# Kernel tuning notes

Measured on AMD Instinct MI355X. Metric: run time of the kernel, lower is better.

Reference implementation:

```python
import jax, jax.numpy as jnp
import numpy as np

B, N, D = 4, 2048, 1024


def setup_inputs() -> dict:
    key = jax.random.key(0)
    ks = jax.random.split(key, 9)
    x = jax.random.normal(ks[0], (B, N, D), dtype=jnp.float32)
    # causal mask: True = masked (set to -inf), per dot_product_attention semantics
    mask = jnp.triu(jnp.ones((N, N), dtype=bool), k=1)
    mask = jnp.broadcast_to(mask, (B, N, N))
    scale = 1.0 / np.sqrt(D)
    Wq = jax.random.normal(ks[1], (D, D), dtype=jnp.float32) * scale
    Wk = jax.random.normal(ks[2], (D, D), dtype=jnp.float32) * scale
    Wv = jax.random.normal(ks[3], (D, D), dtype=jnp.float32) * scale
    Wo = jax.random.normal(ks[4], (D, D), dtype=jnp.float32) * scale
    bq = jnp.zeros((D,), dtype=jnp.float32)
    bk = jnp.zeros((D,), dtype=jnp.float32)
    bv = jnp.zeros((D,), dtype=jnp.float32)
    bo = jnp.zeros((D,), dtype=jnp.float32)
    return {"x": x, "mask": mask, "Wq": Wq, "bq": bq, "Wk": Wk, "bk": bk,
            "Wv": Wv, "bv": bv, "Wo": Wo, "bo": bo}


def reference(x, mask, Wq, bq, Wk, bk, Wv, bv, Wo, bo):
    # QKV projections (single-head despite docstring; module never splits heads)
    Q = x @ Wq + bq  # [b, n, d]
    K = x @ Wk + bk
    V = x @ Wv + bv
    d = K.shape[-1]
    scores = jnp.einsum('bqd,bkd->bqk', Q, K) / jnp.sqrt(jnp.asarray(d, Q.dtype))
    min_infty = jnp.finfo(scores.dtype).min
    scores = jnp.where(mask, min_infty, scores)
    weights = jax.nn.softmax(scores, axis=-1)
    attention = jnp.einsum('bqk,bkd->bqd', weights, V)
    out = attention @ Wo + bo
    return out
```

## Files before the change

### kernel.cpp

```cpp
#include <hip/hip_runtime.h>
#include <hip/hip_bf16.h>

typedef __attribute__((ext_vector_type(8))) short short8;
typedef __attribute__((ext_vector_type(4))) float f32x4;

__device__ inline float b2f(unsigned short u) {
    union { unsigned int i; float f; } c; c.i = ((unsigned int)u) << 16; return c.f;
}
__device__ inline unsigned short f2b(float f) {
    __hip_bfloat16 h = __float2bfloat16(f);
    return *reinterpret_cast<unsigned short*>(&h);
}

__device__ inline void gl_lds16(const unsigned short* g, unsigned short* ldsbase) {
    __builtin_amdgcn_global_load_lds(
        (const __attribute__((address_space(1))) unsigned int*)(g),
        (__attribute__((address_space(3))) unsigned int*)(ldsbase),
        16, 0, 0);
}

__global__ __launch_bounds__(256) void cvt_f32_bf16(
    const float* __restrict__ src, unsigned short* __restrict__ dst, int n4)
{
    int i = blockIdx.x * 256 + threadIdx.x;
    if (i >= n4) return;
    float4 v = ((const float4*)src)[i];
    union { unsigned short u[4]; unsigned long long ll; } p;
    p.u[0] = f2b(v.x); p.u[1] = f2b(v.y); p.u[2] = f2b(v.z); p.u[3] = f2b(v.w);
    ((unsigned long long*)dst)[i] = p.ll;
}

__global__ __launch_bounds__(256) void cvt_weights4(
    const float* __restrict__ s0, const float* __restrict__ s1, const float* __restrict__ s2,
    const float* __restrict__ s3,
    unsigned short* __restrict__ d0, unsigned short* __restrict__ d1,
    unsigned short* __restrict__ d2, unsigned short* __restrict__ d3)
{
    const int z = blockIdx.z;
    if (z == 3) {
        const int i = (blockIdx.y * 32 + blockIdx.x) * 256 + threadIdx.x;
        float4 v = ((const float4*)s3)[i];
        union { unsigned short u[4]; unsigned long long ll; } p;
        p.u[0] = f2b(v.x); p.u[1] = f2b(v.y); p.u[2] = f2b(v.z); p.u[3] = f2b(v.w);
        ((unsigned long long*)d3)[i] = p.ll;
        return;
    }
    const float* src = z == 0 ? s0 : z == 1 ? s1 : s2;
    unsigned short* dst = z == 0 ? d0 : z == 1 ? d1 : d2;
    __shared__ float tile[32][33];
    const int c0 = blockIdx.x * 32, r0 = blockIdx.y * 32;
    const int tx = threadIdx.x & 31, ty = threadIdx.x >> 5;
    #pragma unroll
    for (int i = ty; i < 32; i += 8)
        tile[i][tx] = src[(long)(r0 + i) * 1024 + c0 + tx];
    __syncthreads();
    #pragma unroll
    for (int i = ty; i < 32; i += 8)
        dst[(long)(c0 + i) * 1024 + r0 + tx] = f2b(tile[tx][i]);
}

__global__ __launch_bounds__(64) void make_bvo(
    const unsigned short* __restrict__ Wot, const float* __restrict__ bv,
    const float* __restrict__ bo, float* __restrict__ bvo)
{
    const int n = blockIdx.x;
    const int lane = threadIdx.x;
    const unsigned short* row = Wot + (long)n * 1024;
    float acc = 0.f;
    #pragma unroll
    for (int pass = 0; pass < 2; pass++) {
        const int k = pass * 512 + lane * 8;
        short8 wv = *(const short8*)(row + k);
        #pragma unroll
        for (int j = 0; j < 8; j++)
            acc += bv[k + j] * b2f((unsigned short)wv[j]);
    }
    #pragma unroll
    for (int off = 32; off > 0; off >>= 1) acc += __shfl_xor(acc, off, 64);
    if (lane == 0) bvo[n] = acc + bo[n];
}

#define TILE_DECLS \
    __shared__ __attribute__((aligned(16))) unsigned short As[2 * 128 * 32]; \
    __shared__ __attribute__((aligned(16))) unsigned short Bs[2 * 128 * 32]; \
    const int t = threadIdx.x, lane = t & 63, w = t >> 6; \
    const int wr = w >> 1, wc = w & 1; \
    const int lrow = lane & 15, quad = lane >> 4; \
    f32x4 acc[4][4]; \
    _Pragma("unroll") for (int i = 0; i < 4; i++) \
        _Pragma("unroll") for (int j = 0; j < 4; j++) \
            acc[i][j] = (f32x4){0.f, 0.f, 0.f, 0.f};

#define TILE_KLOOP(gA, lda, gB, ldb, Keff) \
    for (int k0 = 0; k0 < (Keff); k0 += 64) { \
        _Pragma("unroll") for (int p = 0; p < 2; p++) \
            _Pragma("unroll") for (int h = 0; h < 2; h++) { \
                gl_lds16((gA) + (long)h * 16 * (lda) + k0 + p * 32, \
                         &As[p * 4096 + (w * 32 + h * 16) * 32]); \
                gl_lds16((gB) + (long)h * 16 * (ldb) + k0 + p * 32, \
                         &Bs[p * 4096 + (w * 32 + h * 16) * 32]); \
            } \
        __syncthreads(); \
        _Pragma("unroll") for (int p = 0; p < 2; p++) { \
            short8 af[4], bfr[4]; \
            _Pragma("unroll") for (int mi = 0; mi < 4; mi++) \
                af[mi] = *(const short8*)&As[p * 4096 + (wr * 64 + mi * 16 + lrow) * 32 + quad * 8]; \
            _Pragma("unroll") for (int ni = 0; ni < 4; ni++) \
                bfr[ni] = *(const short8*)&Bs[p * 4096 + (wc * 64 + ni * 16 + lrow) * 32 + quad * 8]; \
            _Pragma("unroll") for (int mi = 0; mi < 4; mi++) \
                _Pragma("unroll") for (int ni = 0; ni < 4; ni++) \
                    acc[mi][ni] = __builtin_amdgcn_mfma_f32_16x16x32_bf16( \
                        af[mi], bfr[ni], acc[mi][ni], 0, 0, 0); \
        } \
        __syncthreads(); \
    }

__global__ __launch_bounds__(256) void qkv_proj(
    const unsigned short* __restrict__ A,
    const unsigned short* __restrict__ Wqt, const unsigned short* __restrict__ Wkt,
    const unsigned short* __restrict__ Wvot,
    const float* __restrict__ bq, const float* __restrict__ bk,
    unsigned short* __restrict__ Q, unsigned short* __restrict__ Km,
    unsigned short* __restrict__ Vot)
{
    const int bm = blockIdx.x, bn = blockIdx.y;
    const int r = bn >> 3, bnn = bn & 7;
    const unsigned short* Bt = (r == 0) ? Wqt : (r == 1) ? Wkt : Wvot;
    const float* bias = (r == 0) ? bq : (r == 1) ? bk : nullptr;
    const int m0 = bm * 128, n0 = bnn * 128;

    TILE_DECLS

    const unsigned short* gA = A  + (long)(m0 + w * 32 + (lane >> 2)) * 1024 + (lane & 3) * 8;
    const unsigned short* gB = Bt + (long)(n0 + w * 32 + (lane >> 2)) * 1024 + (lane & 3) * 8;
    TILE_KLOOP(gA, 1024, gB, 1024, 1024)

    #pragma unroll
    for (int mi = 0; mi < 4; mi++) {
        const int m = m0 + wr * 64 + mi * 16 + quad * 4;
        #pragma unroll
        for (int ni = 0; ni < 4; ni++) {
            const int n = n0 + wc * 64 + ni * 16 + lrow;
            const float bvl = bias ? bias[n] : 0.f;
            if (r < 2) {
                unsigned short* out = (r == 0) ? Q : Km;
                #pragma unroll
                for (int rg = 0; rg < 4; rg++)
                    out[(long)(m + rg) * 1024 + n] = f2b(acc[mi][ni][rg] + bvl);
            } else {
                #pragma unroll
                for (int rg = 0; rg < 4; rg++)
                    Vot[(long)n * 8192 + m + rg] = f2b(acc[mi][ni][rg]);
            }
        }
    }
}

template<bool TRI, bool KCAUSAL, int OMODE>
__global__ __launch_bounds__(256) void gemm128(
    const unsigned short* __restrict__ A, const unsigned short* __restrict__ Bt,
    const float* __restrict__ bias, void* __restrict__ Cv,
    int K, int lda, int ldb, int ldc, long sA, long sB, long sC, float scale)
{
    int bm, bn, bz;
    if (TRI) {
        const int q = blockIdx.x;
        bm = (int)((sqrtf(8.f * q + 1.f) - 1.f) * 0.5f);
        while ((bm + 1) * (bm + 2) / 2 <= q) bm++;
        while (bm * (bm + 1) / 2 > q) bm--;
        bn = q - bm * (bm + 1) / 2;
        bz = blockIdx.y;
    } else {
        bm = KCAUSAL ? (gridDim.x - 1 - blockIdx.x) : blockIdx.x;
        bn = blockIdx.y; bz = blockIdx.z;
    }
    A  += (long)bz * sA;
    Bt += (long)bz * sB;
    const int m0 = bm * 128, n0 = bn * 128;

    TILE_DECLS

    const int Keff = KCAUSAL ? ((bm + 1) * 128 < K ? (bm + 1) * 128 : K) : K;
    const unsigned short* gA = A  + (long)(m0 + w * 32 + (lane >> 2)) * lda + (lane & 3) * 8;
    const unsigned short* gB = Bt + (long)(n0 + w * 32 + (lane >> 2)) * ldb + (lane & 3) * 8;
    TILE_KLOOP(gA, lda, gB, ldb, Keff)

    #pragma unroll
    for (int mi = 0; mi < 4; mi++) {
        const int m = m0 + wr * 64 + mi * 16 + quad * 4;
        #pragma unroll
        for (int ni = 0; ni < 4; ni++) {
            const int n = n0 + wc * 64 + ni * 16 + lrow;
            const float bvl = bias ? bias[n] : 0.f;
            #pragma unroll
            for (int rg = 0; rg < 4; rg++) {
                const float val = acc[mi][ni][rg] * scale + bvl;
                if (OMODE == 1)
                    ((float*)Cv)[(long)bz * sC + (long)(m + rg) * ldc + n] = val;
                else
                    ((unsigned short*)Cv)[(long)bz * sC + (long)(m + rg) * ldc + n] = f2b(val);
            }
        }
    }
}

__global__ __launch_bounds__(256) void softmax_causal(unsigned short* __restrict__ S)
{
    const long row = blockIdx.x;
    const int i = (int)(row & 2047);
    unsigned short* base = S + row * 2048;
    const int t = threadIdx.x;
    const int padded = ((i >> 7) + 1) << 7;
    const int j0 = t * 8;
    const bool active = j0 < padded;

    __shared__ float red[4];

    float v[8];
    if (active) {
        short8 s8 = *(const short8*)(base + j0);
        #pragma unroll
        for (int jj = 0; jj < 8; jj++)
            v[jj] = (j0 + jj <= i) ? b2f((unsigned short)s8[jj]) : -3.0e38f;
    } else {
        #pragma unroll
        for (int jj = 0; jj < 8; jj++) v[jj] = -3.0e38f;
    }

    float lmax = v[0];
    #pragma unroll
    for (int jj = 1; jj < 8; jj++) lmax = fmaxf(lmax, v[jj]);
    #pragma unroll
    for (int off = 32; off > 0; off >>= 1) lmax = fmaxf(lmax, __shfl_xor(lmax, off, 64));
    if ((t & 63) == 0) red[t >> 6] = lmax;
    __syncthreads();
    const float gmax = fmaxf(fmaxf(red[0], red[1]), fmaxf(red[2], red[3]));
    __syncthreads();

    float lsum = 0.f;
    #pragma unroll
    for (int jj = 0; jj < 8; jj++) {
        v[jj] = (v[jj] > -1.0e37f) ? __expf(v[jj] - gmax) : 0.f;
        lsum += v[jj];
    }
    #pragma unroll
    for (int off = 32; off > 0; off >>= 1) lsum += __shfl_xor(lsum, off, 64);
    if ((t & 63) == 0) red[t >> 6] = lsum;
    __syncthreads();
    const float inv = 1.0f / (red[0] + red[1] + red[2] + red[3]);

    if (active) {
        short8 p8;
        #pragma unroll
        for (int jj = 0; jj < 8; jj++) p8[jj] = (short)f2b(v[jj] * inv);
        *(short8*)(base + j0) = p8;
    }
}

extern "C" void kernel_launch(void* const* d_in, const int* in_sizes, int n_in,
                              void* d_out, int out_size, void* d_ws, size_t ws_size,
                              hipStream_t stream)
{
    const float* x  = (const float*)d_in[0];
    const float* Wq = (const float*)d_in[2];
    const float* bq = (const float*)d_in[3];
    const float* Wk = (const float*)d_in[4];
    const float* bk = (const float*)d_in[5];
    const float* Wv = (const float*)d_in[6];
    const float* bv = (const float*)d_in[7];
    const float* Wo = (const float*)d_in[8];
    const float* bo = (const float*)d_in[9];

    unsigned short* ws = (unsigned short*)d_ws;
    const long XSZ = 8192L * 1024;
    const long WSZ = 1024L * 1024;
    unsigned short* xb   = ws;
    unsigned short* Wqt  = ws + XSZ;
    unsigned short* Wkt  = Wqt + WSZ;
    unsigned short* Wot  = Wkt + WSZ;
    unsigned short* Wvb  = Wot + WSZ;
    unsigned short* Wvot = Wvb + WSZ;
    unsigned short* Q    = Wvot + WSZ;
    unsigned short* Km   = Q + XSZ;
    unsigned short* Vot  = Km + XSZ;
    unsigned short* S    = Vot + XSZ;
    float*          bvo  = (float*)(S + 4L * 2048 * 2048);

    const dim3 blk(256);

    cvt_f32_bf16<<<dim3(8192), blk, 0, stream>>>(x, xb, (int)(XSZ / 4));
    cvt_weights4<<<dim3(32, 32, 4), blk, 0, stream>>>(
        Wq, Wk, Wo, Wv, Wqt, Wkt, Wot, Wvb);
    make_bvo    <<<dim3(1024), dim3(64), 0, stream>>>(Wot, bv, bo, bvo);

    gemm128<false, false, 0><<<dim3(8, 8, 1), blk, 0, stream>>>(
        Wot, Wvb, nullptr, Wvot, 1024, 1024, 1024, 1024, 0, 0, 0, 1.f);

    qkv_proj<<<dim3(64, 24), blk, 0, stream>>>(
        xb, Wqt, Wkt, Wvot, bq, bk, Q, Km, Vot);

    gemm128<true, false, 0><<<dim3(136, 4), blk, 0, stream>>>(
        Q, Km, nullptr, S, 1024, 1024, 1024, 2048,
        2048L * 1024, 2048L * 1024, 2048L * 2048, 0.03125f);

    softmax_causal<<<dim3(4 * 2048), blk, 0, stream>>>(S);

    gemm128<false, true, 1><<<dim3(16, 8, 4), blk, 0, stream>>>(
        S, Vot, bvo, (float*)d_out, 2048, 2048, 8192, 1024,
        2048L * 2048, 2048, 2048L * 1024, 1.f);
}
```

Before: 341.9 us.

## Replace 128-tile GEMMs with 256x256 tiles using swizzled LDS and fine-grained pipeline

Introduces a 512-thread GEMM that computes 256x256 output tiles. It uses an XOR-swizzled, double-buffered LDS layout and a software pipeline that interleaves async global-to-LDS loads with MFMA phases, explicit waitcnt/barrier scheduling and setprio. The QKV projection, the causal score GEMM and the PV GEMM all switch to it, and the softmax padding granularity moves to 256 to match. Larger tiles raise data reuse and cut LDS bank conflicts, but produce fewer blocks (e.g. 144 for scores, 128 for PV), which risks underfilling the GPU and wastes more work on the causal diagonal.

New measurement: 352.2 us. 3.0% more time.

```diff
diff --git a/kernel.cpp b/kernel.cpp
--- a/kernel.cpp
+++ b/kernel.cpp
@@ -115,47 +115,6 @@
         __syncthreads(); \
     }
 
-__global__ __launch_bounds__(256) void qkv_proj(
-    const unsigned short* __restrict__ A,
-    const unsigned short* __restrict__ Wqt, const unsigned short* __restrict__ Wkt,
-    const unsigned short* __restrict__ Wvot,
-    const float* __restrict__ bq, const float* __restrict__ bk,
-    unsigned short* __restrict__ Q, unsigned short* __restrict__ Km,
-    unsigned short* __restrict__ Vot)
-{
-    const int bm = blockIdx.x, bn = blockIdx.y;
-    const int r = bn >> 3, bnn = bn & 7;
-    const unsigned short* Bt = (r == 0) ? Wqt : (r == 1) ? Wkt : Wvot;
-    const float* bias = (r == 0) ? bq : (r == 1) ? bk : nullptr;
-    const int m0 = bm * 128, n0 = bnn * 128;
-
-    TILE_DECLS
-
-    const unsigned short* gA = A  + (long)(m0 + w * 32 + (lane >> 2)) * 1024 + (lane & 3) * 8;
-    const unsigned short* gB = Bt + (long)(n0 + w * 32 + (lane >> 2)) * 1024 + (lane & 3) * 8;
-    TILE_KLOOP(gA, 1024, gB, 1024, 1024)
-
-    #pragma unroll
-    for (int mi = 0; mi < 4; mi++) {
-        const int m = m0 + wr * 64 + mi * 16 + quad * 4;
-        #pragma unroll
-        for (int ni = 0; ni < 4; ni++) {
-            const int n = n0 + wc * 64 + ni * 16 + lrow;
-            const float bvl = bias ? bias[n] : 0.f;
-            if (r < 2) {
-                unsigned short* out = (r == 0) ? Q : Km;
-                #pragma unroll
-                for (int rg = 0; rg < 4; rg++)
-                    out[(long)(m + rg) * 1024 + n] = f2b(acc[mi][ni][rg] + bvl);
-            } else {
-                #pragma unroll
-                for (int rg = 0; rg < 4; rg++)
-                    Vot[(long)n * 8192 + m + rg] = f2b(acc[mi][ni][rg]);
-            }
-        }
-    }
-}
-
 template<bool TRI, bool KCAUSAL, int OMODE>
 __global__ __launch_bounds__(256) void gemm128(
     const unsigned short* __restrict__ A, const unsigned short* __restrict__ Bt,
@@ -204,13 +163,183 @@
     }
 }
 
+
+#define G256_SHARED \
+    __shared__ __attribute__((aligned(16))) unsigned short As[2][256 * 64]; \
+    __shared__ __attribute__((aligned(16))) unsigned short Bs[2][256 * 64];
+
+#define G256_DECLS(Aptr, Bptr, LDA, LDB) \
+    const int tid = threadIdx.x, lane = tid & 63, w = tid >> 6; \
+    const int wm = w >> 2, wn = w & 3; \
+    const int lrow = lane & 15, quad = lane >> 4; \
+    const int srow = lane >> 3; \
+    const int scol = ((lane & 7) ^ srow) << 3; \
+    const int lda_ = (LDA), ldb_ = (LDB); \
+    const unsigned short* gA = (Aptr) + (long)(m0 + srow) * lda_ + scol; \
+    const unsigned short* gB = (Bptr) + (long)(n0 + srow) * ldb_ + scol; \
+    f32x4 acc[8][4]; \
+    _Pragma("unroll") for (int i_ = 0; i_ < 8; i_++) \
+        _Pragma("unroll") for (int j_ = 0; j_ < 4; j_++) \
+            acc[i_][j_] = (f32x4){0.f, 0.f, 0.f, 0.f}; \
+    short8 af[4][2], bf[2][2];
+
+#define G256_STAGE(pr, kt, b) { \
+    _Pragma("unroll") for (int j_ = 0; j_ < 2; j_++) { \
+        const int row_ = ((pr) & 1) * 128 + j_ * 64 + w * 8; \
+        if ((pr) < 2) gl_lds16(gA + (long)row_ * lda_ + (long)(kt) * 64, &As[(b)][row_ * 64]); \
+        else          gl_lds16(gB + (long)row_ * ldb_ + (long)(kt) * 64, &Bs[(b)][row_ * 64]); \
+    } }
+
+#define G256_RA(MH, P) \
+    _Pragma("unroll") for (int i_ = 0; i_ < 4; i_++) \
+        _Pragma("unroll") for (int k_ = 0; k_ < 2; k_++) \
+            af[i_][k_] = *(const short8*)&As[(P)][(wm * 128 + ((MH) * 4 + i_) * 16 + lrow) * 64 \
+                                                 + (((k_ * 4 + quad) ^ (lrow & 7)) << 3)];
+#define G256_RB(NH, P) \
+    _Pragma("unroll") for (int j_ = 0; j_ < 2; j_++) \
+        _Pragma("unroll") for (int k_ = 0; k_ < 2; k_++) \
+            bf[j_][k_] = *(const short8*)&Bs[(P)][(wn * 64 + ((NH) * 2 + j_) * 16 + lrow) * 64 \
+                                                 + (((k_ * 4 + quad) ^ (lrow & 7)) << 3)];
+#define G256_MFMA(MH, NH) \
+    _Pragma("unroll") for (int k_ = 0; k_ < 2; k_++) \
+        _Pragma("unroll") for (int i_ = 0; i_ < 4; i_++) \
+            _Pragma("unroll") for (int j_ = 0; j_ < 2; j_++) \
+                acc[(MH) * 4 + i_][(NH) * 2 + j_] = __builtin_amdgcn_mfma_f32_16x16x32_bf16( \
+                    af[i_][k_], bf[j_][k_], acc[(MH) * 4 + i_][(NH) * 2 + j_], 0, 0, 0);
+
+#define G256_RUN(NT) { \
+    G256_STAGE(0, 0, 0) G256_STAGE(1, 0, 0) G256_STAGE(2, 0, 0) G256_STAGE(3, 0, 0) \
+    if ((NT) > 1) { \
+        G256_STAGE(0, 1, 1) G256_STAGE(1, 1, 1) \
+        asm volatile("s_waitcnt vmcnt(4)" ::: "memory"); \
+    } else { \
+        asm volatile("s_waitcnt vmcnt(0)" ::: "memory"); \
+    } \
+    __builtin_amdgcn_s_barrier(); \
+    for (int tt = 0; tt < (NT); tt++) { \
+        const int p_ = tt & 1; \
+        const bool s1_ = (tt + 1 < (NT)), s2_ = (tt + 2 < (NT)); \
+        G256_RA(0, p_) G256_RB(0, p_) \
+        if (s1_) G256_STAGE(2, tt + 1, p_ ^ 1) \
+        __builtin_amdgcn_s_barrier(); \
+        __builtin_amdgcn_s_setprio(1); G256_MFMA(0, 0) __builtin_amdgcn_s_setprio(0); \
+        asm volatile("s_waitcnt lgkmcnt(0)" ::: "memory"); \
+        __builtin_amdgcn_s_barrier(); \
+        G256_RB(1, p_) \
+        if (s1_) G256_STAGE(3, tt + 1, p_ ^ 1) \
+        __builtin_amdgcn_s_barrier(); \
+        __builtin_amdgcn_s_setprio(1); G256_MFMA(0, 1) __builtin_amdgcn_s_setprio(0); \
+        asm volatile("s_waitcnt lgkmcnt(0)" ::: "memory"); \
+        __builtin_amdgcn_s_barrier(); \
+        G256_RA(1, p_) \
+        __builtin_amdgcn_s_barrier(); \
+        __builtin_amdgcn_s_setprio(1); G256_MFMA(1, 1) __builtin_amdgcn_s_setprio(0); \
+        asm volatile("s_waitcnt lgkmcnt(0)" ::: "memory"); \
+        __builtin_amdgcn_s_barrier(); \
+        G256_RB(0, p_) \
+        if (s2_) { G256_STAGE(0, tt + 2, p_) G256_STAGE(1, tt + 2, p_) } \
+        __builtin_amdgcn_s_barrier(); \
+        __builtin_amdgcn_s_setprio(1); G256_MFMA(1, 0) __builtin_amdgcn_s_setprio(0); \
+        asm volatile("s_waitcnt lgkmcnt(0)" ::: "memory"); \
+        if (s2_) { asm volatile("s_waitcnt vmcnt(4)" ::: "memory"); } \
+        else     { asm volatile("s_waitcnt vmcnt(0)" ::: "memory"); } \
+        __builtin_amdgcn_s_barrier(); \
+        __builtin_amdgcn_sched_barrier(0); \
+    } }
+
+template<bool TRI, bool KCAUSAL, int OMODE>
+__global__ __launch_bounds__(512, 2) void gemm256(
+    const unsigned short* __restrict__ A, const unsigned short* __restrict__ Bt,
+    const float* __restrict__ bias, void* __restrict__ Cv,
+    int K, int lda, int ldb, int ldc, long sA, long sB, long sC, float scale)
+{
+    G256_SHARED
+    int bm, bn, bz;
+    if (TRI) {
+        const int q = blockIdx.x;
+        bm = (int)((sqrtf(8.f * q + 1.f) - 1.f) * 0.5f);
+        while ((bm + 1) * (bm + 2) / 2 <= q) bm++;
+        while (bm * (bm + 1) / 2 > q) bm--;
+        bn = q - bm * (bm + 1) / 2;
+        bz = blockIdx.y;
+    } else {
+        bm = KCAUSAL ? (gridDim.x - 1 - (int)blockIdx.x) : blockIdx.x;
+        bn = blockIdx.y; bz = blockIdx.z;
+    }
+    A  += (long)bz * sA;
+    Bt += (long)bz * sB;
+    const int m0 = bm * 256, n0 = bn * 256;
+    const int Keff = KCAUSAL ? ((bm + 1) * 256 < K ? (bm + 1) * 256 : K) : K;
+    const int nt = Keff >> 6;
+
+    G256_DECLS(A, Bt, lda, ldb)
+    G256_RUN(nt)
+
+    #pragma unroll
+    for (int mi = 0; mi < 8; mi++) {
+        const int m = m0 + wm * 128 + mi * 16 + quad * 4;
+        #pragma unroll
+        for (int ni = 0; ni < 4; ni++) {
+            const int n = n0 + wn * 64 + ni * 16 + lrow;
+            const float bvl = bias ? bias[n] : 0.f;
+            #pragma unroll
+            for (int rg = 0; rg < 4; rg++) {
+                const float val = acc[mi][ni][rg] * scale + bvl;
+                if (OMODE == 1)
+                    ((float*)Cv)[(long)bz * sC + (long)(m + rg) * ldc + n] = val;
+                else
+                    ((unsigned short*)Cv)[(long)bz * sC + (long)(m + rg) * ldc + n] = f2b(val);
+            }
+        }
+    }
+}
+
+__global__ __launch_bounds__(512, 2) void qkv256(
+    const unsigned short* __restrict__ A,
+    const unsigned short* __restrict__ Wqt, const unsigned short* __restrict__ Wkt,
+    const unsigned short* __restrict__ Wvot,
+    const float* __restrict__ bq, const float* __restrict__ bk,
+    unsigned short* __restrict__ Q, unsigned short* __restrict__ Km,
+    unsigned short* __restrict__ Vot)
+{
+    G256_SHARED
+    const int bm = blockIdx.x, by = blockIdx.y;
+    const int r = by >> 2, bnn = by & 3;
+    const unsigned short* Bt = (r == 0) ? Wqt : (r == 1) ? Wkt : Wvot;
+    const float* bias = (r == 0) ? bq : (r == 1) ? bk : nullptr;
+    const int m0 = bm * 256, n0 = bnn * 256;
+
+    G256_DECLS(A, Bt, 1024, 1024)
+    G256_RUN(16)
+
+    #pragma unroll
+    for (int mi = 0; mi < 8; mi++) {
+        const int m = m0 + wm * 128 + mi * 16 + quad * 4;
+        #pragma unroll
+        for (int ni = 0; ni < 4; ni++) {
+            const int n = n0 + wn * 64 + ni * 16 + lrow;
+            if (r < 2) {
+                unsigned short* out = (r == 0) ? Q : Km;
+                const float bvl = bias[n];
+                #pragma unroll
+                for (int rg = 0; rg < 4; rg++)
+                    out[(long)(m + rg) * 1024 + n] = f2b(acc[mi][ni][rg] + bvl);
+            } else {
+                #pragma unroll
+                for (int rg = 0; rg < 4; rg++)
+                    Vot[(long)n * 8192 + m + rg] = f2b(acc[mi][ni][rg]);
+            }
+        }
+    }
+}
+
 __global__ __launch_bounds__(256) void softmax_causal(unsigned short* __restrict__ S)
 {
     const long row = blockIdx.x;
     const int i = (int)(row & 2047);
     unsigned short* base = S + row * 2048;
     const int t = threadIdx.x;
-    const int padded = ((i >> 7) + 1) << 7;
+    const int padded = ((i >> 8) + 1) << 8;
     const int j0 = t * 8;
     const bool active = j0 < padded;
 
@@ -296,16 +425,16 @@
     gemm128<false, false, 0><<<dim3(8, 8, 1), blk, 0, stream>>>(
         Wot, Wvb, nullptr, Wvot, 1024, 1024, 1024, 1024, 0, 0, 0, 1.f);
 
-    qkv_proj<<<dim3(64, 24), blk, 0, stream>>>(
+    qkv256<<<dim3(32, 12), dim3(512), 0, stream>>>(
         xb, Wqt, Wkt, Wvot, bq, bk, Q, Km, Vot);
 
-    gemm128<true, false, 0><<<dim3(136, 4), blk, 0, stream>>>(
+    gemm256<true, false, 0><<<dim3(36, 4), dim3(512), 0, stream>>>(
         Q, Km, nullptr, S, 1024, 1024, 1024, 2048,
         2048L * 1024, 2048L * 1024, 2048L * 2048, 0.03125f);
 
     softmax_causal<<<dim3(4 * 2048), blk, 0, stream>>>(S);
 
-    gemm128<false, true, 1><<<dim3(16, 8, 4), blk, 0, stream>>>(
+    gemm256<false, true, 1><<<dim3(8, 4, 4), dim3(512), 0, stream>>>(
         S, Vot, bvo, (float*)d_out, 2048, 2048, 8192, 1024,
         2048L * 2048, 2048, 2048L * 1024, 1.f);
 }
```

## Replace QKV projection with 256x256-tile, 8-wave pipelined GEMM kernel

Applied to the files above, without the earlier changes.

Swaps the 128x128 QKV projection kernel for a new 256x256-tile kernel using 512 threads, double-buffered LDS with direct global-to-LDS loads, an XOR-swizzled LDS layout, and interleaved prefetch and MFMA phases with s_setprio. Larger tiles raise arithmetic intensity and cut global reloads of the activation and weight matrices. The swizzle is meant to remove LDS bank conflicts and the phased barriers to overlap loads with matrix math. The cost is much higher register and LDS use per block (128 KB of LDS) and fewer blocks in the grid (384 instead of 1536), which may hurt occupancy and load balance.

Result: no change. 345.5 us (+1.1%).

```diff
diff --git a/kernel.cpp b/kernel.cpp
--- a/kernel.cpp
+++ b/kernel.cpp
@@ -115,47 +115,6 @@
         __syncthreads(); \
     }
 
-__global__ __launch_bounds__(256) void qkv_proj(
-    const unsigned short* __restrict__ A,
-    const unsigned short* __restrict__ Wqt, const unsigned short* __restrict__ Wkt,
-    const unsigned short* __restrict__ Wvot,
-    const float* __restrict__ bq, const float* __restrict__ bk,
-    unsigned short* __restrict__ Q, unsigned short* __restrict__ Km,
-    unsigned short* __restrict__ Vot)
-{
-    const int bm = blockIdx.x, bn = blockIdx.y;
-    const int r = bn >> 3, bnn = bn & 7;
-    const unsigned short* Bt = (r == 0) ? Wqt : (r == 1) ? Wkt : Wvot;
-    const float* bias = (r == 0) ? bq : (r == 1) ? bk : nullptr;
-    const int m0 = bm * 128, n0 = bnn * 128;
-
-    TILE_DECLS
-
-    const unsigned short* gA = A  + (long)(m0 + w * 32 + (lane >> 2)) * 1024 + (lane & 3) * 8;
-    const unsigned short* gB = Bt + (long)(n0 + w * 32 + (lane >> 2)) * 1024 + (lane & 3) * 8;
-    TILE_KLOOP(gA, 1024, gB, 1024, 1024)
-
-    #pragma unroll
-    for (int mi = 0; mi < 4; mi++) {
-        const int m = m0 + wr * 64 + mi * 16 + quad * 4;
-        #pragma unroll
-        for (int ni = 0; ni < 4; ni++) {
-            const int n = n0 + wc * 64 + ni * 16 + lrow;
-            const float bvl = bias ? bias[n] : 0.f;
-            if (r < 2) {
-                unsigned short* out = (r == 0) ? Q : Km;
-                #pragma unroll
-                for (int rg = 0; rg < 4; rg++)
-                    out[(long)(m + rg) * 1024 + n] = f2b(acc[mi][ni][rg] + bvl);
-            } else {
-                #pragma unroll
-                for (int rg = 0; rg < 4; rg++)
-                    Vot[(long)n * 8192 + m + rg] = f2b(acc[mi][ni][rg]);
-            }
-        }
-    }
-}
-
 template<bool TRI, bool KCAUSAL, int OMODE>
 __global__ __launch_bounds__(256) void gemm128(
     const unsigned short* __restrict__ A, const unsigned short* __restrict__ Bt,
@@ -199,6 +158,120 @@
                     ((float*)Cv)[(long)bz * sC + (long)(m + rg) * ldc + n] = val;
                 else
                     ((unsigned short*)Cv)[(long)bz * sC + (long)(m + rg) * ldc + n] = f2b(val);
+            }
+        }
+    }
+}
+
+
+#define G256_DECLS(Aptr, Bptr, LDA, LDB) \
+    const int tid = threadIdx.x, lane = tid & 63, w = tid >> 6; \
+    const int wm = w >> 2, wn = w & 3; \
+    const int lrow = lane & 15, quad = lane >> 4; \
+    const int srow = lane >> 3; \
+    const int scol = ((lane & 7) ^ srow) << 3; \
+    const int lda_ = (LDA), ldb_ = (LDB); \
+    const unsigned short* gA = (Aptr) + (long)(m0 + srow) * lda_ + scol; \
+    const unsigned short* gB = (Bptr) + (long)(n0 + srow) * ldb_ + scol; \
+    f32x4 acc[8][4]; \
+    _Pragma("unroll") for (int i_ = 0; i_ < 8; i_++) \
+        _Pragma("unroll") for (int j_ = 0; j_ < 4; j_++) \
+            acc[i_][j_] = (f32x4){0.f, 0.f, 0.f, 0.f}; \
+    short8 af[4][2], bf[2][2];
+
+#define G256_STAGE(pr, kt, b) { \
+    _Pragma("unroll") for (int j_ = 0; j_ < 2; j_++) { \
+        const int row_ = ((pr) & 1) * 128 + j_ * 64 + w * 8; \
+        if ((pr) < 2) gl_lds16(gA + (long)row_ * lda_ + (long)(kt) * 64, &As[(b)][row_ * 64]); \
+        else          gl_lds16(gB + (long)row_ * ldb_ + (long)(kt) * 64, &Bs[(b)][row_ * 64]); \
+    } }
+
+#define G256_RA(MH, P) \
+    _Pragma("unroll") for (int i_ = 0; i_ < 4; i_++) \
+        _Pragma("unroll") for (int k_ = 0; k_ < 2; k_++) \
+            af[i_][k_] = *(const short8*)&As[(P)][(wm * 128 + ((MH) * 4 + i_) * 16 + lrow) * 64 \
+                                                 + (((k_ * 4 + quad) ^ (lrow & 7)) << 3)];
+#define G256_RB(NH, P) \
+    _Pragma("unroll") for (int j_ = 0; j_ < 2; j_++) \
+        _Pragma("unroll") for (int k_ = 0; k_ < 2; k_++) \
+            bf[j_][k_] = *(const short8*)&Bs[(P)][(wn * 64 + ((NH) * 2 + j_) * 16 + lrow) * 64 \
+                                                 + (((k_ * 4 + quad) ^ (lrow & 7)) << 3)];
+#define G256_MFMA(MH, NH) \
+    _Pragma("unroll") for (int k_ = 0; k_ < 2; k_++) \
+        _Pragma("unroll") for (int i_ = 0; i_ < 4; i_++) \
+            _Pragma("unroll") for (int j_ = 0; j_ < 2; j_++) \
+                acc[(MH) * 4 + i_][(NH) * 2 + j_] = __builtin_amdgcn_mfma_f32_16x16x32_bf16( \
+                    af[i_][k_], bf[j_][k_], acc[(MH) * 4 + i_][(NH) * 2 + j_], 0, 0, 0);
+
+#define G256_TILE(P, tt) { \
+    const bool pf_ = (tt) + 1 < 16; \
+    G256_RA(0, P) G256_RB(0, P) \
+    if (pf_) { G256_STAGE(0, (tt) + 1, (P) ^ 1) G256_STAGE(1, (tt) + 1, (P) ^ 1) } \
+    __builtin_amdgcn_s_barrier(); \
+    __builtin_amdgcn_s_setprio(1); G256_MFMA(0, 0) __builtin_amdgcn_s_setprio(0); \
+    __builtin_amdgcn_s_barrier(); \
+    G256_RB(1, P) \
+    if (pf_) { G256_STAGE(2, (tt) + 1, (P) ^ 1) G256_STAGE(3, (tt) + 1, (P) ^ 1) } \
+    __builtin_amdgcn_s_barrier(); \
+    __builtin_amdgcn_s_setprio(1); G256_MFMA(0, 1) __builtin_amdgcn_s_setprio(0); \
+    __builtin_amdgcn_s_barrier(); \
+    G256_RA(1, P) \
+    __builtin_amdgcn_s_barrier(); \
+    __builtin_amdgcn_s_setprio(1); G256_MFMA(1, 1) __builtin_amdgcn_s_setprio(0); \
+    __builtin_amdgcn_s_barrier(); \
+    G256_RB(0, P) \
+    __builtin_amdgcn_s_barrier(); \
+    __builtin_amdgcn_s_setprio(1); G256_MFMA(1, 0) __builtin_amdgcn_s_setprio(0); \
+    asm volatile("s_waitcnt lgkmcnt(0)"); \
+    asm volatile("s_waitcnt vmcnt(0)"); \
+    __builtin_amdgcn_s_barrier(); \
+}
+
+__global__ __launch_bounds__(512, 2) void qkv256(
+    const unsigned short* __restrict__ A,
+    const unsigned short* __restrict__ Wqt, const unsigned short* __restrict__ Wkt,
+    const unsigned short* __restrict__ Wvot,
+    const float* __restrict__ bq, const float* __restrict__ bk,
+    unsigned short* __restrict__ Q, unsigned short* __restrict__ Km,
+    unsigned short* __restrict__ Vot)
+{
+    __shared__ __attribute__((aligned(16))) unsigned short As[2][256 * 64];
+    __shared__ __attribute__((aligned(16))) unsigned short Bs[2][256 * 64];
+
+    const int bm = blockIdx.x, by = blockIdx.y;
+    const int r = by >> 2, bnn = by & 3;
+    const unsigned short* Bt = (r == 0) ? Wqt : (r == 1) ? Wkt : Wvot;
+    const float* bias = (r == 0) ? bq : (r == 1) ? bk : nullptr;
+    const int m0 = bm * 256, n0 = bnn * 256;
+
+    G256_DECLS(A, Bt, 1024, 1024)
+
+    G256_STAGE(0, 0, 0) G256_STAGE(1, 0, 0) G256_STAGE(2, 0, 0) G256_STAGE(3, 0, 0)
+    asm volatile("s_waitcnt vmcnt(0)");
+    __builtin_amdgcn_s_barrier();
+
+    #pragma unroll 1
+    for (int tt = 0; tt < 16; tt += 2) {
+        G256_TILE(0, tt)
+        G256_TILE(1, tt + 1)
+    }
+
+    #pragma unroll
+    for (int mi = 0; mi < 8; mi++) {
+        const int m = m0 + wm * 128 + mi * 16 + quad * 4;
+        #pragma unroll
+        for (int ni = 0; ni < 4; ni++) {
+            const int n = n0 + wn * 64 + ni * 16 + lrow;
+            if (r < 2) {
+                unsigned short* out = (r == 0) ? Q : Km;
+                const float bvl = bias[n];
+                #pragma unroll
+                for (int rg = 0; rg < 4; rg++)
+                    out[(long)(m + rg) * 1024 + n] = f2b(acc[mi][ni][rg] + bvl);
+            } else {
+                #pragma unroll
+                for (int rg = 0; rg < 4; rg++)
+                    Vot[(long)n * 8192 + m + rg] = f2b(acc[mi][ni][rg]);
             }
         }
     }
@@ -296,7 +369,7 @@
     gemm128<false, false, 0><<<dim3(8, 8, 1), blk, 0, stream>>>(
         Wot, Wvb, nullptr, Wvot, 1024, 1024, 1024, 1024, 0, 0, 0, 1.f);
 
-    qkv_proj<<<dim3(64, 24), blk, 0, stream>>>(
+    qkv256<<<dim3(32, 12), dim3(512), 0, stream>>>(
         xb, Wqt, Wkt, Wvot, bq, bk, Q, Km, Vot);
 
     gemm128<true, false, 0><<<dim3(136, 4), blk, 0, stream>>>(
```

## Merge prep kernels into one launch and stage QKV epilogue stores through LDS

Applied to the files above, without the earlier changes.

Folds the x conversion, the weight transpose/convert and the bvo bias precompute into a single prep kernel. This removes two launches, and bvo is now computed straight from fp32 Wo instead of waiting on the transposed copy. The qkv_proj epilogue now writes results into LDS first: Q/K go out as row-major 16-byte vector stores, and the transposed V tile uses an XOR swizzle before vectorised stores. This replaces the scattered 2-byte global stores. The cost is an extra barrier and LDS traffic in the epilogue, and most prep blocks in the z=6 slice exit immediately.

New measurement: 338.4 us. About the same (-1.0%).

```diff
diff --git a/kernel.cpp b/kernel.cpp
--- a/kernel.cpp
+++ b/kernel.cpp
@@ -19,70 +19,99 @@
         16, 0, 0);
 }
 
-__global__ __launch_bounds__(256) void cvt_f32_bf16(
-    const float* __restrict__ src, unsigned short* __restrict__ dst, int n4)
-{
-    int i = blockIdx.x * 256 + threadIdx.x;
-    if (i >= n4) return;
-    float4 v = ((const float4*)src)[i];
-    union { unsigned short u[4]; unsigned long long ll; } p;
-    p.u[0] = f2b(v.x); p.u[1] = f2b(v.y); p.u[2] = f2b(v.z); p.u[3] = f2b(v.w);
-    ((unsigned long long*)dst)[i] = p.ll;
-}
-
-__global__ __launch_bounds__(256) void cvt_weights4(
-    const float* __restrict__ s0, const float* __restrict__ s1, const float* __restrict__ s2,
-    const float* __restrict__ s3,
-    unsigned short* __restrict__ d0, unsigned short* __restrict__ d1,
-    unsigned short* __restrict__ d2, unsigned short* __restrict__ d3)
+__global__ __launch_bounds__(256) void prep(
+    const float* __restrict__ x,
+    const float* __restrict__ Wq, const float* __restrict__ Wk,
+    const float* __restrict__ Wo, const float* __restrict__ Wv,
+    const float* __restrict__ bv, const float* __restrict__ bo,
+    unsigned short* __restrict__ xb,
+    unsigned short* __restrict__ Wqt, unsigned short* __restrict__ Wkt,
+    unsigned short* __restrict__ Wot, unsigned short* __restrict__ Wvb,
+    float* __restrict__ bvo)
 {
     const int z = blockIdx.z;
+    const int t = threadIdx.x;
+    __shared__ float tile[32][33];
+
+    if (z < 3) {
+        const float* src = z == 0 ? Wq : z == 1 ? Wk : Wo;
+        unsigned short* dst = z == 0 ? Wqt : z == 1 ? Wkt : Wot;
+        const int c0 = blockIdx.x * 32, r0 = blockIdx.y * 32;
+        const int tx = t & 31, ty = t >> 5;
+        #pragma unroll
+        for (int i = ty; i < 32; i += 8)
+            tile[i][tx] = src[(long)(r0 + i) * 1024 + c0 + tx];
+        __syncthreads();
+        #pragma unroll
+        for (int i = ty; i < 32; i += 8)
+            dst[(long)(c0 + i) * 1024 + r0 + tx] = f2b(tile[tx][i]);
+        return;
+    }
     if (z == 3) {
-        const int i = (blockIdx.y * 32 + blockIdx.x) * 256 + threadIdx.x;
-        float4 v = ((const float4*)s3)[i];
+        const int i = (blockIdx.y * 32 + blockIdx.x) * 256 + t;
+        float4 v = ((const float4*)Wv)[i];
         union { unsigned short u[4]; unsigned long long ll; } p;
         p.u[0] = f2b(v.x); p.u[1] = f2b(v.y); p.u[2] = f2b(v.z); p.u[3] = f2b(v.w);
-        ((unsigned long long*)d3)[i] = p.ll;
+        ((unsigned long long*)Wvb)[i] = p.ll;
         return;
     }
-    const float* src = z == 0 ? s0 : z == 1 ? s1 : s2;
-    unsigned short* dst = z == 0 ? d0 : z == 1 ? d1 : d2;
-    __shared__ float tile[32][33];
-    const int c0 = blockIdx.x * 32, r0 = blockIdx.y * 32;
-    const int tx = threadIdx.x & 31, ty = threadIdx.x >> 5;
-    #pragma unroll
-    for (int i = ty; i < 32; i += 8)
-        tile[i][tx] = src[(long)(r0 + i) * 1024 + c0 + tx];
+    if (z < 6) {
+        const int bl = (z - 4) * 1024 + blockIdx.y * 32 + blockIdx.x;
+        #pragma unroll
+        for (int k = 0; k < 4; k++) {
+            const int i = bl * 1024 + k * 256 + t;
+            float4 v = ((const float4*)x)[i];
+            union { unsigned short u[4]; unsigned long long ll; } p;
+            p.u[0] = f2b(v.x); p.u[1] = f2b(v.y); p.u[2] = f2b(v.z); p.u[3] = f2b(v.w);
+            ((unsigned long long*)xb)[i] = p.ll;
+        }
+        return;
+    }
+    if (blockIdx.y != 0) return;
+    const int tx = t & 31, ty = t >> 5;
+    const int n = blockIdx.x * 32 + tx;
+    float acc = 0.f;
+    #pragma unroll 4
+    for (int j = 0; j < 128; j++) {
+        const int k = ty * 128 + j;
+        acc += Wo[(long)k * 1024 + n] * bv[k];
+    }
+    float* red = &tile[0][0];
+    red[ty * 32 + tx] = acc;
     __syncthreads();
-    #pragma unroll
-    for (int i = ty; i < 32; i += 8)
-        dst[(long)(c0 + i) * 1024 + r0 + tx] = f2b(tile[tx][i]);
-}
-
-__global__ __launch_bounds__(64) void make_bvo(
-    const unsigned short* __restrict__ Wot, const float* __restrict__ bv,
-    const float* __restrict__ bo, float* __restrict__ bvo)
-{
-    const int n = blockIdx.x;
-    const int lane = threadIdx.x;
-    const unsigned short* row = Wot + (long)n * 1024;
-    float acc = 0.f;
-    #pragma unroll
-    for (int pass = 0; pass < 2; pass++) {
-        const int k = pass * 512 + lane * 8;
-        short8 wv = *(const short8*)(row + k);
-        #pragma unroll
-        for (int j = 0; j < 8; j++)
-            acc += bv[k + j] * b2f((unsigned short)wv[j]);
-    }
-    #pragma unroll
-    for (int off = 32; off > 0; off >>= 1) acc += __shfl_xor(acc, off, 64);
-    if (lane == 0) bvo[n] = acc + bo[n];
-}
+    if (ty == 0) {
+        float s = 0.f;
+        #pragma unroll
+        for (int j = 0; j < 8; j++) s += red[j * 32 + tx];
+        bvo[n] = s + bo[n];
+    }
+}
+
+#define TILE_KLOOP(As, Bs, gA, lda, gB, ldb, Keff) \
+    for (int k0 = 0; k0 < (Keff); k0 += 64) { \
+        _Pragma("unroll") for (int p = 0; p < 2; p++) \
+            _Pragma("unroll") for (int h = 0; h < 2; h++) { \
+                gl_lds16((gA) + (long)h * 16 * (lda) + k0 + p * 32, \
+                         &(As)[p * 4096 + (w * 32 + h * 16) * 32]); \
+                gl_lds16((gB) + (long)h * 16 * (ldb) + k0 + p * 32, \
+                         &(Bs)[p * 4096 + (w * 32 + h * 16) * 32]); \
+            } \
+        __syncthreads(); \
+        _Pragma("unroll") for (int p = 0; p < 2; p++) { \
+            short8 af[4], bfr[4]; \
+            _Pragma("unroll") for (int mi = 0; mi < 4; mi++) \
+                af[mi] = *(const short8*)&(As)[p * 4096 + (wr * 64 + mi * 16 + lrow) * 32 + quad * 8]; \
+            _Pragma("unroll") for (int ni = 0; ni < 4; ni++) \
+                bfr[ni] = *(const short8*)&(Bs)[p * 4096 + (wc * 64 + ni * 16 + lrow) * 32 + quad * 8]; \
+            _Pragma("unroll") for (int mi = 0; mi < 4; mi++) \
+                _Pragma("unroll") for (int ni = 0; ni < 4; ni++) \
+                    acc[mi][ni] = __builtin_amdgcn_mfma_f32_16x16x32_bf16( \
+                        af[mi], bfr[ni], acc[mi][ni], 0, 0, 0); \
+        } \
+        __syncthreads(); \
+    }
 
 #define TILE_DECLS \
-    __shared__ __attribute__((aligned(16))) unsigned short As[2 * 128 * 32]; \
-    __shared__ __attribute__((aligned(16))) unsigned short Bs[2 * 128 * 32]; \
     const int t = threadIdx.x, lane = t & 63, w = t >> 6; \
     const int wr = w >> 1, wc = w & 1; \
     const int lrow = lane & 15, quad = lane >> 4; \
@@ -91,77 +120,14 @@
         _Pragma("unroll") for (int j = 0; j < 4; j++) \
             acc[i][j] = (f32x4){0.f, 0.f, 0.f, 0.f};
 
-#define TILE_KLOOP(gA, lda, gB, ldb, Keff) \
-    for (int k0 = 0; k0 < (Keff); k0 += 64) { \
-        _Pragma("unroll") for (int p = 0; p < 2; p++) \
-            _Pragma("unroll") for (int h = 0; h < 2; h++) { \
-                gl_lds16((gA) + (long)h * 16 * (lda) + k0 + p * 32, \
-                         &As[p * 4096 + (w * 32 + h * 16) * 32]); \
-                gl_lds16((gB) + (long)h * 16 * (ldb) + k0 + p * 32, \
-                         &Bs[p * 4096 + (w * 32 + h * 16) * 32]); \
-            } \
-        __syncthreads(); \
-        _Pragma("unroll") for (int p = 0; p < 2; p++) { \
-            short8 af[4], bfr[4]; \
-            _Pragma("unroll") for (int mi = 0; mi < 4; mi++) \
-                af[mi] = *(const short8*)&As[p * 4096 + (wr * 64 + mi * 16 + lrow) * 32 + quad * 8]; \
-            _Pragma("unroll") for (int ni = 0; ni < 4; ni++) \
-                bfr[ni] = *(const short8*)&Bs[p * 4096 + (wc * 64 + ni * 16 + lrow) * 32 + quad * 8]; \
-            _Pragma("unroll") for (int mi = 0; mi < 4; mi++) \
-                _Pragma("unroll") for (int ni = 0; ni < 4; ni++) \
-                    acc[mi][ni] = __builtin_amdgcn_mfma_f32_16x16x32_bf16( \
-                        af[mi], bfr[ni], acc[mi][ni], 0, 0, 0); \
-        } \
-        __syncthreads(); \
-    }
-
-__global__ __launch_bounds__(256) void qkv_proj(
-    const unsigned short* __restrict__ A,
-    const unsigned short* __restrict__ Wqt, const unsigned short* __restrict__ Wkt,
-    const unsigned short* __restrict__ Wvot,
-    const float* __restrict__ bq, const float* __restrict__ bk,
-    unsigned short* __restrict__ Q, unsigned short* __restrict__ Km,
-    unsigned short* __restrict__ Vot)
-{
-    const int bm = blockIdx.x, bn = blockIdx.y;
-    const int r = bn >> 3, bnn = bn & 7;
-    const unsigned short* Bt = (r == 0) ? Wqt : (r == 1) ? Wkt : Wvot;
-    const float* bias = (r == 0) ? bq : (r == 1) ? bk : nullptr;
-    const int m0 = bm * 128, n0 = bnn * 128;
-
-    TILE_DECLS
-
-    const unsigned short* gA = A  + (long)(m0 + w * 32 + (lane >> 2)) * 1024 + (lane & 3) * 8;
-    const unsigned short* gB = Bt + (long)(n0 + w * 32 + (lane >> 2)) * 1024 + (lane & 3) * 8;
-    TILE_KLOOP(gA, 1024, gB, 1024, 1024)
-
-    #pragma unroll
-    for (int mi = 0; mi < 4; mi++) {
-        const int m = m0 + wr * 64 + mi * 16 + quad * 4;
-        #pragma unroll
-        for (int ni = 0; ni < 4; ni++) {
-            const int n = n0 + wc * 64 + ni * 16 + lrow;
-            const float bvl = bias ? bias[n] : 0.f;
-            if (r < 2) {
-                unsigned short* out = (r == 0) ? Q : Km;
-                #pragma unroll
-                for (int rg = 0; rg < 4; rg++)
-                    out[(long)(m + rg) * 1024 + n] = f2b(acc[mi][ni][rg] + bvl);
-            } else {
-                #pragma unroll
-                for (int rg = 0; rg < 4; rg++)
-                    Vot[(long)n * 8192 + m + rg] = f2b(acc[mi][ni][rg]);
-            }
-        }
-    }
-}
-
 template<bool TRI, bool KCAUSAL, int OMODE>
 __global__ __launch_bounds__(256) void gemm128(
     const unsigned short* __restrict__ A, const unsigned short* __restrict__ Bt,
     const float* __restrict__ bias, void* __restrict__ Cv,
     int K, int lda, int ldb, int ldc, long sA, long sB, long sC, float scale)
 {
+    __shared__ __attribute__((aligned(16))) unsigned short As[2 * 128 * 32];
+    __shared__ __attribute__((aligned(16))) unsigned short Bs[2 * 128 * 32];
     int bm, bn, bz;
     if (TRI) {
         const int q = blockIdx.x;
@@ -183,7 +149,7 @@
     const int Keff = KCAUSAL ? ((bm + 1) * 128 < K ? (bm + 1) * 128 : K) : K;
     const unsigned short* gA = A  + (long)(m0 + w * 32 + (lane >> 2)) * lda + (lane & 3) * 8;
     const unsigned short* gB = Bt + (long)(n0 + w * 32 + (lane >> 2)) * ldb + (lane & 3) * 8;
-    TILE_KLOOP(gA, lda, gB, ldb, Keff)
+    TILE_KLOOP(As, Bs, gA, lda, gB, ldb, Keff)
 
     #pragma unroll
     for (int mi = 0; mi < 4; mi++) {
@@ -200,6 +166,77 @@
                 else
                     ((unsigned short*)Cv)[(long)bz * sC + (long)(m + rg) * ldc + n] = f2b(val);
             }
+        }
+    }
+}
+
+__global__ __launch_bounds__(256) void qkv_proj(
+    const unsigned short* __restrict__ A,
+    const unsigned short* __restrict__ Wqt, const unsigned short* __restrict__ Wkt,
+    const unsigned short* __restrict__ Wvot,
+    const float* __restrict__ bq, const float* __restrict__ bk,
+    unsigned short* __restrict__ Q, unsigned short* __restrict__ Km,
+    unsigned short* __restrict__ Vot)
+{
+    __shared__ __attribute__((aligned(16))) unsigned short pool[16384];
+    unsigned short* As = pool;
+    unsigned short* Bs = pool + 8192;
+
+    const int bm = blockIdx.x, by = blockIdx.y;
+    const int r = by >> 3, bnn = by & 7;
+    const unsigned short* Bt = (r == 0) ? Wqt : (r == 1) ? Wkt : Wvot;
+    const float* bias = (r == 0) ? bq : (r == 1) ? bk : nullptr;
+    const int m0 = bm * 128, n0 = bnn * 128;
+
+    TILE_DECLS
+
+    const unsigned short* gA = A  + (long)(m0 + w * 32 + (lane >> 2)) * 1024 + (lane & 3) * 8;
+    const unsigned short* gB = Bt + (long)(n0 + w * 32 + (lane >> 2)) * 1024 + (lane & 3) * 8;
+    TILE_KLOOP(As, Bs, gA, 1024, gB, 1024, 1024)
+
+    if (r < 2) {
+        #pragma unroll
+        for (int mi = 0; mi < 4; mi++) {
+            #pragma unroll
+            for (int ni = 0; ni < 4; ni++) {
+                const int n_l = wc * 64 + ni * 16 + lrow;
+                const float bvl = bias[n0 + n_l];
+                #pragma unroll
+                for (int rg = 0; rg < 4; rg++) {
+                    const int m_l = wr * 64 + mi * 16 + quad * 4 + rg;
+                    pool[m_l * 128 + n_l] = f2b(acc[mi][ni][rg] + bvl);
+                }
+            }
+        }
+        __syncthreads();
+        unsigned short* out = (r == 0) ? Q : Km;
+        #pragma unroll
+        for (int it = 0; it < 8; it++) {
+            const int idx = it * 256 + t;
+            const int m_l = idx >> 4, c = idx & 15;
+            short8 v = *(const short8*)&pool[m_l * 128 + c * 8];
+            *(short8*)&out[(long)(m0 + m_l) * 1024 + n0 + c * 8] = v;
+        }
+    } else {
+        #pragma unroll
+        for (int mi = 0; mi < 4; mi++) {
+            #pragma unroll
+            for (int ni = 0; ni < 4; ni++) {
+                const int n_l = wc * 64 + ni * 16 + lrow;
+                const int mb = wr * 64 + mi * 16 + quad * 4;
+                union { unsigned short u[4]; unsigned long long ll; } pk;
+                #pragma unroll
+                for (int rg = 0; rg < 4; rg++) pk.u[rg] = f2b(acc[mi][ni][rg]);
+                *(unsigned long long*)&pool[n_l * 128 + (mb ^ ((n_l & 15) << 3))] = pk.ll;
+            }
+        }
+        __syncthreads();
+        #pragma unroll
+        for (int it = 0; it < 8; it++) {
+            const int idx = it * 256 + t;
+            const int n_l = idx >> 4, c = idx & 15;
+            short8 v = *(const short8*)&pool[n_l * 128 + ((c * 8) ^ ((n_l & 15) << 3))];
+            *(short8*)&Vot[(long)(n0 + n_l) * 8192 + m0 + c * 8] = v;
         }
     }
 }
@@ -288,10 +325,8 @@
 
     const dim3 blk(256);
 
-    cvt_f32_bf16<<<dim3(8192), blk, 0, stream>>>(x, xb, (int)(XSZ / 4));
-    cvt_weights4<<<dim3(32, 32, 4), blk, 0, stream>>>(
-        Wq, Wk, Wo, Wv, Wqt, Wkt, Wot, Wvb);
-    make_bvo    <<<dim3(1024), dim3(64), 0, stream>>>(Wot, bv, bo, bvo);
+    prep<<<dim3(32, 32, 7), blk, 0, stream>>>(
+        x, Wq, Wk, Wo, Wv, bv, bo, xb, Wqt, Wkt, Wot, Wvb, bvo);
 
     gemm128<false, false, 0><<<dim3(8, 8, 1), blk, 0, stream>>>(
         Wot, Wvb, nullptr, Wvot, 1024, 1024, 1024, 1024, 0, 0, 0, 1.f);
```
